# Kernel optimization log

Measured on AMD Instinct MI355X. Metric: run time of the kernel, lower is better.

## Reference

```python
import jax, jax.numpy as jnp
import numpy as np

B, C, T, H, W = 4, 256, 8, 28, 28
IC = 128  # inter_channels = in_channels // 2


def setup_inputs() -> dict:
    key = jax.random.key(0)
    ks = jax.random.split(key, 5)
    s_in = 1.0 / np.sqrt(C)
    s_ic = 1.0 / np.sqrt(IC)
    return {
        "x": jax.random.normal(ks[0], (B, C, T, H, W), dtype=jnp.float32),
        "Wg": jax.random.normal(ks[1], (IC, C), dtype=jnp.float32) * s_in,
        "Wtheta": jax.random.normal(ks[2], (IC, C), dtype=jnp.float32) * s_in,
        "Wphi": jax.random.normal(ks[3], (IC, C), dtype=jnp.float32) * s_in,
        "Wz": jax.random.normal(ks[4], (C, IC), dtype=jnp.float32) * s_ic,
    }


def reference(x, Wg, Wtheta, Wphi, Wz):
    b, c, t, h, w = x.shape
    n = t * h * w
    xf = x.reshape(b, c, n)  # 1x1x1 conv == channel GEMM over flattened positions
    g_x = jnp.einsum("oc,bcn->bon", Wg, xf)       # [B, IC, N]
    theta_x = jnp.einsum("oc,bcn->bon", Wtheta, xf)
    phi_x = jnp.einsum("oc,bcn->bon", Wphi, xf)
    # f = theta^T @ phi : [B, N, N]
    f = jnp.einsum("bcn,bcm->bnm", theta_x, phi_x)
    f_div_C = jax.nn.softmax(f, axis=-1)
    # y = f_div_C @ g^T : [B, N, IC] -> keep as [B, IC, N]
    y = jnp.einsum("bnm,bcm->bcn", f_div_C, g_x)  # [B, IC, N]
    z = jnp.einsum("oc,bcn->bon", Wz, y).reshape(b, c, t, h, w) + x
    return z
```

## Files before the change

kernel.cpp:

```cpp
#include <hip/hip_runtime.h>
#include <cstdint>


#define BB   4
#define CCH  256
#define NPOS 6272
#define ICH  128
#define BNIC ((size_t)BB * NPOS * ICH)
#define TKF  32
#define SLACK 12.0f

typedef __attribute__((ext_vector_type(8)))  _Float16 h8v;
typedef __attribute__((ext_vector_type(16))) float fx16;

__device__ __forceinline__ unsigned short f2h(float f) {
  _Float16 h = (_Float16)f;
  return __builtin_bit_cast(unsigned short, h);
}
__device__ __forceinline__ unsigned int pkh(float lo, float hi) {
  return __builtin_bit_cast(unsigned int, __builtin_amdgcn_cvt_pkrtz(lo, hi));
}
__device__ __forceinline__ float h2f(unsigned short u) {
  return (float)__builtin_bit_cast(_Float16, u);
}
__device__ __forceinline__ int vgoff(int dr, int c) {
  return (dr * 4 + (c ^ ((dr >> 1) & 3))) * 8;
}

__global__ __launch_bounds__(256, 1)
void wconv(const float* __restrict__ Wtheta, const float* __restrict__ Wphi,
           const float* __restrict__ Wg,
           unsigned short* __restrict__ Whi, unsigned short* __restrict__ Wlo) {
  const int idx4 = (blockIdx.x * 256 + threadIdx.x) * 4;
  const int p = idx4 >> 15;
  const float* W = (p == 0) ? Wtheta : (p == 1) ? Wphi : Wg;
  const float4 v = *(const float4*)&W[idx4 - (p << 15)];
  const float vv[4] = {v.x, v.y, v.z, v.w};
  ushort4 h, l;
  unsigned short* hp = (unsigned short*)&h;
  unsigned short* lp = (unsigned short*)&l;
  #pragma unroll
  for (int q = 0; q < 4; ++q) {
    _Float16 hh = (_Float16)vv[q];
    hp[q] = __builtin_bit_cast(unsigned short, hh);
    lp[q] = f2h(vv[q] - (float)hh);
  }
  *(ushort4*)&Whi[idx4] = h;
  *(ushort4*)&Wlo[idx4] = l;
}

__global__ __launch_bounds__(256, 2)
void proj_mfma(const float* __restrict__ x,
               const unsigned short* __restrict__ Whi,
               const unsigned short* __restrict__ Wlo,
               unsigned short* __restrict__ Qg,
               unsigned short* __restrict__ Kg,
               unsigned short* __restrict__ Vtg) {
  __shared__ unsigned short Xhi[32][40];
  __shared__ unsigned short Xlo[32][40];
  const int n0 = blockIdx.x * 32;
  const int b  = blockIdx.y;
  const int tid = threadIdx.x;
  const int lane = tid & 63, wv = tid >> 6;
  const int ln = lane & 31, g = lane >> 5;

  fx16 acc[3];
  acc[0] = (fx16)(0.0f); acc[1] = (fx16)(0.0f); acc[2] = (fx16)(0.0f);

  const int sn = tid & 31, cq = (tid >> 5) * 4;
  const float* xp = x + ((size_t)b * CCH + cq) * NPOS + n0 + sn;

  float pv[4];
  #pragma unroll
  for (int q = 0; q < 4; ++q) pv[q] = xp[(size_t)q * NPOS];

  for (int c0 = 0; c0 < CCH; c0 += 32) {
    {
      ushort4 h4, l4;
      unsigned short* hp = (unsigned short*)&h4;
      unsigned short* lp = (unsigned short*)&l4;
      #pragma unroll
      for (int q = 0; q < 4; ++q) {
        _Float16 hh = (_Float16)pv[q];
        hp[q] = __builtin_bit_cast(unsigned short, hh);
        lp[q] = f2h(pv[q] - (float)hh);
      }
      *(ushort4*)&Xhi[sn][cq] = h4;
      *(ushort4*)&Xlo[sn][cq] = l4;
    }
    if (c0 + 32 < CCH) {
      #pragma unroll
      for (int q = 0; q < 4; ++q) pv[q] = xp[(size_t)(c0 + 32 + q) * NPOS];
    }
    __syncthreads();
    #pragma unroll
    for (int kc = 0; kc < 2; ++kc) {
      const h8v bxh = *(const h8v*)&Xhi[ln][kc * 16 + g * 8];
      const h8v bxl = *(const h8v*)&Xlo[ln][kc * 16 + g * 8];
      #pragma unroll
      for (int t = 0; t < 3; ++t) {
        const int T = wv * 3 + t;
        const size_t wb = ((size_t)(T * 32 + ln)) * CCH + c0 + kc * 16 + g * 8;
        const h8v ah = *(const h8v*)&Whi[wb];
        const h8v al = *(const h8v*)&Wlo[wb];
        acc[t] = __builtin_amdgcn_mfma_f32_32x32x16_f16(ah, bxh, acc[t], 0, 0, 0);
        acc[t] = __builtin_amdgcn_mfma_f32_32x32x16_f16(ah, bxl, acc[t], 0, 0, 0);
        acc[t] = __builtin_amdgcn_mfma_f32_32x32x16_f16(al, bxh, acc[t], 0, 0, 0);
      }
    }
    __syncthreads();
  }

  const float LOG2E = 1.4426950408889634f;
  const int n = n0 + ln;
  #pragma unroll
  for (int t = 0; t < 3; ++t) {
    const int T = wv * 3 + t;
    const int p = T >> 2;
    const int ot = (T & 3) * 32;
    if (p < 2) {
      unsigned short* Out = (p == 0) ? Qg : Kg;
      const float scl = (p == 0) ? LOG2E : 1.0f;
      #pragma unroll
      for (int q = 0; q < 4; ++q) {
        ushort4 v;
        v.x = f2h(acc[t][4 * q + 0] * scl);
        v.y = f2h(acc[t][4 * q + 1] * scl);
        v.z = f2h(acc[t][4 * q + 2] * scl);
        v.w = f2h(acc[t][4 * q + 3] * scl);
        *(ushort4*)&Out[((size_t)b * NPOS + n) * ICH + ot + 8 * q + 4 * g] = v;
      }
    } else {
      #pragma unroll
      for (int r = 0; r < 16; ++r) {
        const int o = ot + (r & 3) + 8 * (r >> 2) + 4 * g;
        Vtg[((size_t)b * ICH + o) * NPOS + n] = f2h(acc[t][r]);
      }
    }
  }
}

template <int KS>
__global__ __launch_bounds__(256, 3)
void flash_t(const unsigned short* __restrict__ Qg,
             const unsigned short* __restrict__ Kg,
             const unsigned short* __restrict__ Vtg,
             unsigned short* __restrict__ Opart,
             float* __restrict__ Mpart,
             float* __restrict__ Lpart) {
  constexpr int KLEN = NPOS / KS;
  constexpr int NIT  = KLEN / TKF;
  __shared__ unsigned short Ks[2][TKF * 128];
  __shared__ unsigned short Vs[2][128 * 32];

  const int b   = blockIdx.z;
  const int spl = blockIdx.y;
  const int n0  = blockIdx.x * 128;
  const int kb  = spl * KLEN;
  const int tid = threadIdx.x;
  const int lane = tid & 63, wv = tid >> 6;
  const int qlane = lane & 31, g = lane >> 5;
  const int swz = qlane & 15;

  h8v qf[8];
  {
    const size_t qbase = ((size_t)b * NPOS + n0 + 32 * wv + qlane) * ICH;
    #pragma unroll
    for (int cs = 0; cs < 8; ++cs)
      qf[cs] = *(const h8v*)&Qg[qbase + cs * 16 + g * 8];
  }

  {
    #pragma unroll
    for (int i = 0; i < 2; ++i) {
      const int kr = (tid >> 4) + i * 16, c = tid & 15;
      const uint4 v = *(const uint4*)&Kg[((size_t)b * NPOS + kb + kr) * ICH + c * 8];
      *(uint4*)&Ks[0][kr * 128 + (c ^ (kr & 15)) * 8] = v;
      const int idx = tid * 2 + i, dr = idx >> 2, cv = idx & 3;
      const uint4 w = *(const uint4*)&Vtg[((size_t)b * ICH + dr) * NPOS + kb + cv * 8];
      *(uint4*)&Vs[0][vgoff(dr, cv)] = w;
    }
  }
  __syncthreads();

  float m_run = -1e30f, m_true = -1e30f, l_run = 0.0f;
  fx16 accO[4];
  #pragma unroll
  for (int mt = 0; mt < 4; ++mt) accO[mt] = (fx16)(0.0f);

  uint4 stgK[2], stgV[2];

  for (int it = 0; it < NIT; ++it) {
    const int cur = it & 1;
    const bool pre = (it + 1 < NIT);
    if (pre) {
      const int k0n = kb + (it + 1) * TKF;
      #pragma unroll
      for (int i = 0; i < 2; ++i) {
        const int kr = (tid >> 4) + i * 16;
        stgK[i] = *(const uint4*)&Kg[((size_t)b * NPOS + k0n + kr) * ICH + (tid & 15) * 8];
        const int idx = tid * 2 + i, dr = idx >> 2, cv = idx & 3;
        stgV[i] = *(const uint4*)&Vtg[((size_t)b * ICH + dr) * NPOS + k0n + cv * 8];
      }
    }

    fx16 accS = (fx16)(0.0f);
    #pragma unroll
    for (int cs = 0; cs < 8; ++cs) {
      const h8v aK = *(const h8v*)&Ks[cur][qlane * 128 + ((2 * cs + g) ^ swz) * 8];
      accS = __builtin_amdgcn_mfma_f32_32x32x16_f16(aK, qf[cs], accS, 0, 0, 0);
    }

    float a0 = fmaxf(accS[0], accS[1]),   a1 = fmaxf(accS[2], accS[3]);
    float a2 = fmaxf(accS[4], accS[5]),   a3 = fmaxf(accS[6], accS[7]);
    float a4 = fmaxf(accS[8], accS[9]),   a5 = fmaxf(accS[10], accS[11]);
    float a6 = fmaxf(accS[12], accS[13]), a7 = fmaxf(accS[14], accS[15]);
    a0 = fmaxf(a0, a1); a2 = fmaxf(a2, a3); a4 = fmaxf(a4, a5); a6 = fmaxf(a6, a7);
    float mx = fmaxf(fmaxf(a0, a2), fmaxf(a4, a6));
    mx = fmaxf(mx, __shfl_xor(mx, 32));
    m_true = fmaxf(m_true, mx);
    const bool fold = __any(mx > m_run + SLACK);
    const float mn = fold ? fmaxf(m_run, mx) : m_run;
    float lsum = 0.0f;
    unsigned int pk[4][2];
    #pragma unroll
    for (int u = 0; u < 4; ++u) {
      const float p0 = exp2f(accS[4 * u + 0] - mn);
      const float p1 = exp2f(accS[4 * u + 1] - mn);
      const float p2 = exp2f(accS[4 * u + 2] - mn);
      const float p3 = exp2f(accS[4 * u + 3] - mn);
      lsum += (p0 + p1) + (p2 + p3);
      pk[u][0] = pkh(p0, p1);
      pk[u][1] = pkh(p2, p3);
    }
    lsum += __shfl_xor(lsum, 32);
    if (fold) {
      const float alpha = exp2f(m_run - mn);
      l_run = l_run * alpha + lsum;
      m_run = mn;
      #pragma unroll
      for (int mt = 0; mt < 4; ++mt)
        #pragma unroll
        for (int r = 0; r < 16; ++r) accO[mt][r] *= alpha;
    } else {
      l_run += lsum;
    }

    #pragma unroll
    for (int s = 0; s < 2; ++s) {
      const unsigned int s0 = pk[2 * s + (g ^ 1)][0];
      const unsigned int s1 = pk[2 * s + (g ^ 1)][1];
      const unsigned int t0 = __shfl_xor(s0, 32);
      const unsigned int t1 = __shfl_xor(s1, 32);
      union { unsigned int u[4]; h8v v; } bP;
      bP.u[0] = g ? t0 : pk[2 * s][0];
      bP.u[1] = g ? t1 : pk[2 * s][1];
      bP.u[2] = g ? pk[2 * s + 1][0] : t0;
      bP.u[3] = g ? pk[2 * s + 1][1] : t1;
      #pragma unroll
      for (int mt = 0; mt < 4; ++mt) {
        const h8v aV = *(const h8v*)&Vs[cur][vgoff(32 * mt + qlane, 2 * s + g)];
        accO[mt] = __builtin_amdgcn_mfma_f32_32x32x16_f16(aV, bP.v, accO[mt], 0, 0, 0);
      }
    }

    if (pre) {
      const int nb = cur ^ 1;
      #pragma unroll
      for (int i = 0; i < 2; ++i) {
        const int kr = (tid >> 4) + i * 16;
        *(uint4*)&Ks[nb][kr * 128 + ((tid & 15) ^ (kr & 15)) * 8] = stgK[i];
        const int idx = tid * 2 + i, dr = idx >> 2, cv = idx & 3;
        *(uint4*)&Vs[nb][vgoff(dr, cv)] = stgV[i];
      }
    }
    __syncthreads();
  }

  const float scale = exp2f(m_run - m_true);
  const int ncol = n0 + 32 * wv + qlane;
  const size_t obase = (size_t)(b * KS + spl) * ICH * NPOS;
  #pragma unroll
  for (int mt = 0; mt < 4; ++mt)
    #pragma unroll
    for (int r = 0; r < 16; ++r) {
      const int d = 32 * mt + (r & 3) + 8 * (r >> 2) + 4 * g;
      Opart[obase + (size_t)d * NPOS + ncol] = f2h(accO[mt][r] * scale);
    }
  if (g == 0) {
    Mpart[(size_t)(b * KS + spl) * NPOS + ncol] = m_true;
    Lpart[(size_t)(b * KS + spl) * NPOS + ncol] = l_run * scale;
  }
}

template <int KS>
__global__ __launch_bounds__(256, 2)
void mz_t(const float* __restrict__ x,
          const float* __restrict__ Wz,
          const unsigned short* __restrict__ Opart,
          const float* __restrict__ Mpart,
          const float* __restrict__ Lpart,
          float* __restrict__ out) {
  __shared__ float wgt[64][8];
  __shared__ unsigned short Yh[64][24], Yl[64][24];
  __shared__ unsigned short Wzh[128][24], Wzl[128][24];

  const int n0 = blockIdx.x * 64;
  const int c0 = blockIdx.y * 128;
  const int b  = blockIdx.z;
  const int tid = threadIdx.x;
  const int lane = tid & 63, wv = tid >> 6;
  const int ln = lane & 31, g = lane >> 5;

  if (tid < 64) {
    const int n = n0 + tid;
    float m[KS], l[KS];
    float M0 = -1e30f;
    #pragma unroll
    for (int s = 0; s < KS; ++s) {
      m[s] = Mpart[(size_t)(b * KS + s) * NPOS + n];
      l[s] = Lpart[(size_t)(b * KS + s) * NPOS + n];
      M0 = fmaxf(M0, m[s]);
    }
    float w[KS], lt = 0.0f;
    #pragma unroll
    for (int s = 0; s < KS; ++s) { w[s] = exp2f(m[s] - M0); lt += w[s] * l[s]; }
    const float inv = 1.0f / lt;
    #pragma unroll
    for (int s = 0; s < KS; ++s) wgt[tid][s] = w[s] * inv;
  }
  __syncthreads();

  const int np  = tid & 31;
  const int icg = tid >> 5;
  float wA[KS], wB[KS];
  #pragma unroll
  for (int s = 0; s < KS; ++s) { wA[s] = wgt[2 * np][s]; wB[s] = wgt[2 * np + 1][s]; }
  const int wc = tid >> 1, wh = (tid & 1) * 8;
  const float* Wzrow = Wz + (size_t)(c0 + wc) * ICH + wh;

  fx16 acc[2];
  acc[0] = (fx16)(0.0f); acc[1] = (fx16)(0.0f);

  for (int k0 = 0; k0 < ICH; k0 += 16) {
    {
      const float4 w0 = *(const float4*)&Wzrow[k0];
      const float4 w1 = *(const float4*)&Wzrow[k0 + 4];
      const float wv8[8] = {w0.x, w0.y, w0.z, w0.w, w1.x, w1.y, w1.z, w1.w};
      unsigned int hu[4], lu[4];
      #pragma unroll
      for (int q = 0; q < 4; ++q) {
        _Float16 h0 = (_Float16)wv8[2 * q], h1 = (_Float16)wv8[2 * q + 1];
        hu[q] = (unsigned int)__builtin_bit_cast(unsigned short, h0) |
                ((unsigned int)__builtin_bit_cast(unsigned short, h1) << 16);
        lu[q] = (unsigned int)f2h(wv8[2 * q] - (float)h0) |
                ((unsigned int)f2h(wv8[2 * q + 1] - (float)h1) << 16);
      }
      *(uint4*)&Wzh[wc][wh] = make_uint4(hu[0], hu[1], hu[2], hu[3]);
      *(uint4*)&Wzl[wc][wh] = make_uint4(lu[0], lu[1], lu[2], lu[3]);
    }
    {
      unsigned short h0a[2], h1a[2], l0a[2], l1a[2];
      #pragma unroll
      for (int j = 0; j < 2; ++j) {
        const int ic = k0 + icg * 2 + j;
        float y0 = 0.0f, y1 = 0.0f;
        #pragma unroll
        for (int s = 0; s < KS; ++s) {
          const unsigned int u = *(const unsigned int*)
            &Opart[((size_t)(b * KS + s) * ICH + ic) * NPOS + n0 + 2 * np];
          y0 += wA[s] * h2f((unsigned short)(u & 0xffff));
          y1 += wB[s] * h2f((unsigned short)(u >> 16));
        }
        _Float16 hh0 = (_Float16)y0, hh1 = (_Float16)y1;
        h0a[j] = __builtin_bit_cast(unsigned short, hh0);
        h1a[j] = __builtin_bit_cast(unsigned short, hh1);
        l0a[j] = f2h(y0 - (float)hh0);
        l1a[j] = f2h(y1 - (float)hh1);
      }
      const int kc = icg * 2;
      *(ushort2*)&Yh[2 * np][kc]     = make_ushort2(h0a[0], h0a[1]);
      *(ushort2*)&Yh[2 * np + 1][kc] = make_ushort2(h1a[0], h1a[1]);
      *(ushort2*)&Yl[2 * np][kc]     = make_ushort2(l0a[0], l0a[1]);
      *(ushort2*)&Yl[2 * np + 1][kc] = make_ushort2(l1a[0], l1a[1]);
    }
    __syncthreads();

    const int cr = wv * 32 + ln;
    const h8v Ah = *(const h8v*)&Wzh[cr][g * 8];
    const h8v Al = *(const h8v*)&Wzl[cr][g * 8];
    #pragma unroll
    for (int ni = 0; ni < 2; ++ni) {
      const int nr = ni * 32 + ln;
      const h8v Bh = *(const h8v*)&Yh[nr][g * 8];
      const h8v Bl = *(const h8v*)&Yl[nr][g * 8];
      acc[ni] = __builtin_amdgcn_mfma_f32_32x32x16_f16(Ah, Bh, acc[ni], 0, 0, 0);
      acc[ni] = __builtin_amdgcn_mfma_f32_32x32x16_f16(Ah, Bl, acc[ni], 0, 0, 0);
      acc[ni] = __builtin_amdgcn_mfma_f32_32x32x16_f16(Al, Bh, acc[ni], 0, 0, 0);
    }
    __syncthreads();
  }

  #pragma unroll
  for (int ni = 0; ni < 2; ++ni) {
    const int n = n0 + ni * 32 + ln;
    #pragma unroll
    for (int r = 0; r < 16; ++r) {
      const int c = c0 + wv * 32 + (r & 3) + 8 * (r >> 2) + 4 * g;
      const size_t base = ((size_t)(b * CCH + c)) * NPOS + n;
      out[base] = acc[ni][r] + x[base];
    }
  }
}

extern "C" void kernel_launch(void* const* d_in, const int* in_sizes, int n_in,
                              void* d_out, int out_size, void* d_ws, size_t ws_size,
                              hipStream_t stream) {
  const float* x      = (const float*)d_in[0];
  const float* Wg     = (const float*)d_in[1];
  const float* Wtheta = (const float*)d_in[2];
  const float* Wphi   = (const float*)d_in[3];
  const float* Wz     = (const float*)d_in[4];
  float* out = (float*)d_out;

  unsigned short* Qg    = (unsigned short*)d_ws;
  unsigned short* Kg    = Qg + BNIC;
  unsigned short* Vtg   = Kg + BNIC;
  unsigned short* Opart = Vtg + BNIC;

  unsigned short* Whi = Opart;
  unsigned short* Wlo = Whi + 3 * 128 * 256;

  wconv<<<dim3(96), 256, 0, stream>>>(Wtheta, Wphi, Wg, Whi, Wlo);
  proj_mfma<<<dim3(NPOS / 32, BB), 256, 0, stream>>>(x, Whi, Wlo, Qg, Kg, Vtg);

  const size_t need7 = (3 + 7) * BNIC * 2 + (size_t)2 * 7 * BB * NPOS * 4;
  if (ws_size >= need7) {
    constexpr int KS = 7;
    float* Mpart = (float*)(Opart + (size_t)KS * BNIC);
    float* Lpart = Mpart + (size_t)KS * BB * NPOS;
    flash_t<KS><<<dim3(NPOS / 128, KS, BB), 256, 0, stream>>>(Qg, Kg, Vtg, Opart, Mpart, Lpart);
    mz_t<KS><<<dim3(NPOS / 64, CCH / 128, BB), 256, 0, stream>>>(x, Wz, Opart, Mpart, Lpart, out);
  } else {
    constexpr int KS = 4;
    float* Mpart = (float*)(Opart + (size_t)KS * BNIC);
    float* Lpart = Mpart + (size_t)KS * BB * NPOS;
    flash_t<KS><<<dim3(NPOS / 128, KS, BB), 256, 0, stream>>>(Qg, Kg, Vtg, Opart, Mpart, Lpart);
    mz_t<KS><<<dim3(NPOS / 64, CCH / 128, BB), 256, 0, stream>>>(x, Wz, Opart, Mpart, Lpart, out);
  }
}
```

Before: 282.9 us.

## Stage K/V tiles with direct global-to-LDS loads and raise occupancy bound

```diff
diff --git a/kernel.cpp b/kernel.cpp
--- a/kernel.cpp
+++ b/kernel.cpp
@@ -141,7 +141,7 @@
 }
 
 template <int KS>
-__global__ __launch_bounds__(256, 3)
+__global__ __launch_bounds__(256, 4)
 void flash_t(const unsigned short* __restrict__ Qg,
              const unsigned short* __restrict__ Kg,
              const unsigned short* __restrict__ Vtg,
@@ -170,17 +170,35 @@
       qf[cs] = *(const h8v*)&Qg[qbase + cs * 16 + g * 8];
   }
 
-  {
+  unsigned kOff[2], vOff[2];
+  #pragma unroll
+  for (int i = 0; i < 2; ++i) {
+    const unsigned uoff = (unsigned)(wv * 2 + i) * 512 + (unsigned)lane * 8;
+    const unsigned krow = uoff >> 7, kslot = (uoff >> 3) & 15;
+    const unsigned kgc  = kslot ^ (krow & 15);
+    kOff[i] = (unsigned)(b * NPOS + kb + krow) * ICH + kgc * 8;
+    const unsigned vrow = uoff >> 5;
+    const unsigned vgc  = ((uoff >> 3) & 3) ^ ((uoff >> 6) & 3);
+    vOff[i] = (unsigned)(b * ICH + vrow) * NPOS + kb + vgc * 8;
+  }
+
+  auto STAGE = [&](int bufi) {
     #pragma unroll
     for (int i = 0; i < 2; ++i) {
-      const int kr = (tid >> 4) + i * 16, c = tid & 15;
-      const uint4 v = *(const uint4*)&Kg[((size_t)b * NPOS + kb + kr) * ICH + c * 8];
-      *(uint4*)&Ks[0][kr * 128 + (c ^ (kr & 15)) * 8] = v;
-      const int idx = tid * 2 + i, dr = idx >> 2, cv = idx & 3;
-      const uint4 w = *(const uint4*)&Vtg[((size_t)b * ICH + dr) * NPOS + kb + cv * 8];
-      *(uint4*)&Vs[0][vgoff(dr, cv)] = w;
-    }
-  }
+      __builtin_amdgcn_global_load_lds(
+          (const __attribute__((address_space(1))) void*)&Kg[kOff[i]],
+          (__attribute__((address_space(3))) void*)&Ks[bufi][(wv * 2 + i) * 512],
+          16, 0, 0);
+      __builtin_amdgcn_global_load_lds(
+          (const __attribute__((address_space(1))) void*)&Vtg[vOff[i]],
+          (__attribute__((address_space(3))) void*)&Vs[bufi][(wv * 2 + i) * 512],
+          16, 0, 0);
+      kOff[i] += TKF * ICH;
+      vOff[i] += TKF;
+    }
+  };
+
+  STAGE(0);
   __syncthreads();
 
   float m_run = -1e30f, m_true = -1e30f, l_run = 0.0f;
@@ -188,21 +206,9 @@
   #pragma unroll
   for (int mt = 0; mt < 4; ++mt) accO[mt] = (fx16)(0.0f);
 
-  uint4 stgK[2], stgV[2];
-
   for (int it = 0; it < NIT; ++it) {
     const int cur = it & 1;
-    const bool pre = (it + 1 < NIT);
-    if (pre) {
-      const int k0n = kb + (it + 1) * TKF;
-      #pragma unroll
-      for (int i = 0; i < 2; ++i) {
-        const int kr = (tid >> 4) + i * 16;
-        stgK[i] = *(const uint4*)&Kg[((size_t)b * NPOS + k0n + kr) * ICH + (tid & 15) * 8];
-        const int idx = tid * 2 + i, dr = idx >> 2, cv = idx & 3;
-        stgV[i] = *(const uint4*)&Vtg[((size_t)b * ICH + dr) * NPOS + k0n + cv * 8];
-      }
-    }
+    if (it + 1 < NIT) STAGE(cur ^ 1);
 
     fx16 accS = (fx16)(0.0f);
     #pragma unroll
@@ -264,16 +270,6 @@
       }
     }
 
-    if (pre) {
-      const int nb = cur ^ 1;
-      #pragma unroll
-      for (int i = 0; i < 2; ++i) {
-        const int kr = (tid >> 4) + i * 16;
-        *(uint4*)&Ks[nb][kr * 128 + ((tid & 15) ^ (kr & 15)) * 8] = stgK[i];
-        const int idx = tid * 2 + i, dr = idx >> 2, cv = idx & 3;
-        *(uint4*)&Vs[nb][vgoff(dr, cv)] = stgV[i];
-      }
-    }
     __syncthreads();
   }
 
```

Result: slower. 374.9 us (+32.6%).
